# Kernel tuning notes

Measured on AMD Instinct MI355X. Metric: run time of the kernel, lower is better.

Reference implementation:

```python
import jax, jax.numpy as jnp
import numpy as np

B, S, DIN, DH = 8, 8192, 256, 256


def setup_inputs() -> dict:
    key = jax.random.key(0)
    k0, k1, k2, k3, k4 = jax.random.split(key, 5)
    stdv = 1.0 / np.sqrt(DIN)
    x = jax.random.normal(k0, (B, S, DIN), jnp.float32)
    W0 = jax.random.uniform(k1, (2 * DH, DIN), jnp.float32, -stdv, stdv)
    b0 = jax.random.uniform(k2, (2 * DH,), jnp.float32, -stdv, stdv)
    stdv2 = 1.0 / np.sqrt(DH)
    W1 = jax.random.uniform(k3, (2 * DH, DH), jnp.float32, -stdv2, stdv2)
    b1 = jax.random.uniform(k4, (2 * DH,), jnp.float32, -stdv2, stdv2)
    return {"x": x, "W0": W0, "b0": b0, "W1": W1, "b1": b1}


def _log_g(x):
    # log of g(x) = x + 0.5 for x >= 0 else sigmoid(x)
    return jnp.where(x >= 0, jnp.log(jax.nn.relu(x) + 0.5), -jax.nn.softplus(-x))


def _mingru_layer(x, W, b):
    # x: (B,S,Din); W: (2*DH, Din); b: (2*DH,)
    gh = jnp.einsum('bsd,ed->bse', x, W) + b          # (B,S,2*DH)
    gate, hidden = jnp.split(gh, 2, axis=-1)          # each (B,S,DH)
    log_coeffs = -jax.nn.softplus(gate)               # log(1 - z)
    log_vals = -jax.nn.softplus(-gate) + _log_g(hidden)  # log z + log h_tilde
    Bb, Ss, Dd = log_coeffs.shape
    # initial hidden h0 = g(0) = 0.5  ->  log(h0) = log(0.5)
    log_h0 = jnp.full((Bb, 1, Dd), jnp.log(0.5), log_coeffs.dtype)
    log_values = jnp.concatenate([log_h0, log_vals], axis=1)          # (B,S+1,DH)
    a_star = jnp.concatenate(
        [jnp.zeros((Bb, 1, Dd), log_coeffs.dtype), jnp.cumsum(log_coeffs, axis=1)],
        axis=1)                                                       # (B,S+1,DH)
    log_h = a_star + jax.lax.cumlogsumexp(log_values - a_star, axis=1)
    return jnp.exp(log_h)[:, 1:]                                      # (B,S,DH)


def reference(x, W0, b0, W1, b1):
    out0 = _mingru_layer(x, W0, b0)
    out1 = _mingru_layer(out0, W1, b1)
    h = jnp.stack([out0[:, -1:], out1[:, -1:]])  # (num_layers,B,1,DH)
    return out1, h
```

## Files before the change

kernel.cpp:

```cpp
#include <hip/hip_runtime.h>
#include <hip/hip_bf16.h>

#define Bb 8
#define Ss 8192
#define Dd 256
#define Mm (Bb * Ss)
#define Nn 512
#define NCHUNK 128
#define CLEN (Ss / NCHUNK)
#define TSP 68

typedef __hip_bfloat16 bf16;
typedef __attribute__((ext_vector_type(8))) short short8;
typedef __attribute__((ext_vector_type(4))) float f32x4;

__global__ __launch_bounds__(256) void cvt_weights(
    const float* __restrict__ inA, const float* __restrict__ inB,
    bf16* __restrict__ outA, bf16* __restrict__ outB, long n4each) {
  long i = (long)blockIdx.x * blockDim.x + threadIdx.x;
  const float* in = inA;
  bf16* out = outA;
  if (i >= n4each) {
    in = inB;
    out = outB;
    i -= n4each;
  }
  if (i >= n4each) return;
  const float4 v = ((const float4*)in)[i];
  union { ushort4 u; bf16 h[4]; } o;
  o.h[0] = __float2bfloat16(v.x);
  o.h[1] = __float2bfloat16(v.y);
  o.h[2] = __float2bfloat16(v.z);
  o.h[3] = __float2bfloat16(v.w);
  ((ushort4*)out)[i] = o.u;
}

__device__ __forceinline__ void av_from_gh(float gate, float hid, float& a,
                                           float& v) {
  const float eg = __expf(gate);
  a = __builtin_amdgcn_rcpf(1.f + eg);
  const float z = 1.f - a;
  const float eh = __expf(fminf(hid, 0.f));
  const float sig = eh * __builtin_amdgcn_rcpf(1.f + eh);
  const float gfun = (hid >= 0.f) ? (hid + 0.5f) : sig;
  v = z * gfun;
}

__device__ __forceinline__ unsigned pack_av(float a, float v) {
  union { bf16 h[2]; unsigned u; } o;
  o.h[0] = __float2bfloat16(a);
  o.h[1] = __float2bfloat16(v);
  return o.u;
}

template <bool F32A>
__global__ __launch_bounds__(256, 3) void gemm_av_fused(
    const void* __restrict__ Xv, const bf16* __restrict__ W,
    const float* __restrict__ bias, unsigned* __restrict__ AV,
    float2* __restrict__ AVs) {
  __shared__ __align__(16) char sm[32768];
  bf16* Ab[2] = {(bf16*)sm, (bf16*)(sm + 8192)};
  bf16* Bbf[2] = {(bf16*)(sm + 16384), (bf16*)(sm + 24576)};
  unsigned* Ts = (unsigned*)sm;
  float2* Ps = (float2*)(sm + 20480);

  const int tid = threadIdx.x;
  const int w = tid >> 6;
  const int l = tid & 63;
  const int fl = l & 15;
  const int q = l >> 4;

  const int id = blockIdx.x;
  const int lin = ((id & 7) << 8) | (id >> 3);
  const int cb = lin & 3;
  const int bt = lin >> 2;
  const long rowBase = (long)bt * 128;
  const int wrow = (w >> 1) * 64;
  const int wc = (w & 1) * 32;

  const float* Xf = (const float*)Xv;
  const bf16* Xb = (const bf16*)Xv;

  const float* aSF[2];
  const bf16* aSB[2];
  const bf16* bS[2];
  int ldsOff[2];
#pragma unroll
  for (int c = 0; c < 2; c++) {
    const int idx = c * 256 + tid;
    const int row = idx >> 2;
    const int kq = idx & 3;
    ldsOff[c] = row * 32 + (kq ^ ((row >> 1) & 3)) * 8;
    aSF[c] = Xf + (rowBase + row) * 256 + kq * 8;
    aSB[c] = Xb + (rowBase + row) * 256 + kq * 8;
    const int grow = (row < 64) ? (cb * 64 + row) : (192 + cb * 64 + row);
    bS[c] = W + (long)grow * 256 + kq * 8;
  }

  short8 aReg[2], bReg[2];
  float4 aF[2][2];

  auto loadG = [&](int ks) {
    if constexpr (F32A) {
#pragma unroll
      for (int c = 0; c < 2; c++) {
        aF[c][0] = *(const float4*)(aSF[c] + ks * 32);
        aF[c][1] = *(const float4*)(aSF[c] + ks * 32 + 4);
      }
    } else {
#pragma unroll
      for (int c = 0; c < 2; c++)
        aReg[c] = *(const short8*)(aSB[c] + ks * 32);
    }
#pragma unroll
    for (int c = 0; c < 2; c++)
      bReg[c] = *(const short8*)(bS[c] + ks * 32);
  };
  auto writeL = [&](int bi) {
#pragma unroll
    for (int c = 0; c < 2; c++) {
      short8 av_;
      if constexpr (F32A) {
        const float vals[8] = {aF[c][0].x, aF[c][0].y, aF[c][0].z, aF[c][0].w,
                               aF[c][1].x, aF[c][1].y, aF[c][1].z, aF[c][1].w};
#pragma unroll
        for (int i = 0; i < 8; i++) {
          union { bf16 h; short s; } t;
          t.h = __float2bfloat16(vals[i]);
          av_[i] = t.s;
        }
      } else {
        av_ = aReg[c];
      }
      *(short8*)(Ab[bi] + ldsOff[c]) = av_;
    }
#pragma unroll
    for (int c = 0; c < 2; c++)
      *(short8*)(Bbf[bi] + ldsOff[c]) = bReg[c];
  };

  int aOff[4], bOff[4];
#pragma unroll
  for (int mt = 0; mt < 4; mt++) {
    const int row = wrow + 16 * mt + fl;
    aOff[mt] = row * 32 + (q ^ ((row >> 1) & 3)) * 8;
  }
#pragma unroll
  for (int nt = 0; nt < 4; nt++) {
    const int row =
        (nt < 2) ? (wc + 16 * nt + fl) : (64 + wc + 16 * (nt - 2) + fl);
    bOff[nt] = row * 32 + (q ^ ((row >> 1) & 3)) * 8;
  }

  f32x4 acc[4][4];
#pragma unroll
  for (int i = 0; i < 4; i++)
#pragma unroll
    for (int j = 0; j < 4; j++) acc[i][j] = (f32x4)0.0f;

  loadG(0);
  writeL(0);
  loadG(1);
  __syncthreads();
#pragma unroll
  for (int ks = 0; ks < 8; ks++) {
    const int bi = ks & 1;
    short8 af[4], bf_[4];
#pragma unroll
    for (int mt = 0; mt < 4; mt++)
      af[mt] = *(const short8*)(Ab[bi] + aOff[mt]);
#pragma unroll
    for (int nt = 0; nt < 4; nt++)
      bf_[nt] = *(const short8*)(Bbf[bi] + bOff[nt]);
    if (ks < 7) writeL(bi ^ 1);
    if (ks < 6) loadG(ks + 2);
#pragma unroll
    for (int mt = 0; mt < 4; mt++)
#pragma unroll
      for (int nt = 0; nt < 4; nt++)
        acc[mt][nt] = __builtin_amdgcn_mfma_f32_16x16x32_bf16(
            af[mt], bf_[nt], acc[mt][nt], 0, 0, 0);
    asm volatile("s_waitcnt lgkmcnt(0)" ::: "memory");
    __builtin_amdgcn_s_barrier();
  }

  float bg[2], bh[2];
#pragma unroll
  for (int p = 0; p < 2; p++) {
    const int d = cb * 64 + wc + 16 * p + fl;
    bg[p] = bias[d];
    bh[p] = bias[256 + d];
  }
  unsigned pk[4][2][4];
#pragma unroll
  for (int mt = 0; mt < 4; mt++)
#pragma unroll
    for (int p = 0; p < 2; p++)
#pragma unroll
      for (int r = 0; r < 4; r++) {
        float a, v;
        av_from_gh(acc[mt][p][r] + bg[p], acc[mt][p + 2][r] + bh[p], a, v);
        pk[mt][p][r] = pack_av(a, v);
      }

#pragma unroll
  for (int h = 0; h < 2; h++) {
    if ((w >> 1) == h) {
#pragma unroll
      for (int mt = 0; mt < 4; mt++)
#pragma unroll
        for (int p = 0; p < 2; p++)
#pragma unroll
          for (int r = 0; r < 4; r++)
            Ts[(16 * mt + 4 * q + r) * TSP + wc + 16 * p + fl] = pk[mt][p][r];
    }
    __syncthreads();
    {
      unsigned* dst = AV + ((long)cb * Mm + rowBase + h * 64) * 64;
#pragma unroll
      for (int j = 0; j < 4; j++) {
        const int idx = j * 256 + tid;
        const int t = idx >> 4;
        const int d4 = idx & 15;
        const uint4 val = *(const uint4*)(Ts + t * TSP + d4 * 4);
        *(uint4*)(dst + 4 * idx) = val;
      }
    }
    {
      const int dl = tid & 63;
      const int sg = tid >> 6;
      float A = 1.f, H = 0.f;
#pragma unroll
      for (int t = 0; t < 16; t++) {
        const unsigned p = Ts[(sg * 16 + t) * TSP + dl];
        const float a = __uint_as_float((p & 0xffffu) << 16);
        const float v = __uint_as_float(p & 0xffff0000u);
        A *= a;
        H = a * H + v;
      }
      Ps[sg * 64 + dl] = make_float2(A, H);
    }
    __syncthreads();
    if (tid < 64) {
      float2 r = Ps[tid];
#pragma unroll
      for (int s = 1; s < 4; s++) {
        const float2 n = Ps[s * 64 + tid];
        r = make_float2(r.x * n.x, n.x * r.y + n.y);
      }
      const long cg = (long)(bt >> 6) * NCHUNK + ((bt & 63) << 1) + h;
      AVs[cg * 256 + cb * 64 + tid] = r;
    }
    __syncthreads();
  }
}

template <bool WRITE_BF16>
__global__ __launch_bounds__(256) void scan_final(
    const unsigned* __restrict__ AV, const float2* __restrict__ AVs,
    bf16* __restrict__ OutB, float* __restrict__ OutF,
    float* __restrict__ Hlast) {
  const int d = threadIdx.x;
  const int c = blockIdx.x % NCHUNK;
  const int b = blockIdx.x / NCHUNK;

  float h = 0.5f;
#pragma unroll 4
  for (int j = 0; j < c; j++) {
    const float2 av = AVs[((long)b * NCHUNK + j) * 256 + d];
    h = av.x * h + av.y;
  }

  const long row0 = (long)b * Ss + (long)c * CLEN;
  const unsigned* src = AV + (long)(d >> 6) * Mm * 64 + (d & 63);
  long obase = row0 * 256 + d;
#pragma unroll 8
  for (int t = 0; t < CLEN; t++) {
    const unsigned p = src[(row0 + t) * 64];
    const float a = __uint_as_float((p & 0xffffu) << 16);
    const float v = __uint_as_float(p & 0xffff0000u);
    h = a * h + v;
    if (WRITE_BF16)
      OutB[obase] = __float2bfloat16(h);
    else
      OutF[obase] = h;
    obase += 256;
  }
  if (c == NCHUNK - 1) Hlast[b * 256 + d] = h;
}

extern "C" void kernel_launch(void* const* d_in, const int* in_sizes, int n_in,
                              void* d_out, int out_size, void* d_ws,
                              size_t ws_size, hipStream_t stream) {
  const float* x = (const float*)d_in[0];
  const float* W0f = (const float*)d_in[1];
  const float* b0 = (const float*)d_in[2];
  const float* W1f = (const float*)d_in[3];
  const float* b1 = (const float*)d_in[4];

  float* outF = (float*)d_out;
  float* hlast = outF + (long)Mm * 256;
  bf16* X1b = (bf16*)d_out;

  char* ws = (char*)d_ws;
  unsigned* AV = (unsigned*)ws;
  bf16* W0b = (bf16*)(ws + (long)Mm * 256 * 4);
  bf16* W1b = W0b + (long)Nn * Dd;
  float2* AVs = (float2*)(W1b + (long)Nn * Dd);

  const dim3 gemmGrid(2048);
  const dim3 blk(256);

  const long n4w = (long)Nn * Dd / 4;
  cvt_weights<<<dim3((2 * n4w + 255) / 256), blk, 0, stream>>>(W0f, W1f, W0b,
                                                               W1b, n4w);

  gemm_av_fused<true><<<gemmGrid, blk, 0, stream>>>(x, W0b, b0, AV, AVs);
  scan_final<true><<<dim3(Bb * NCHUNK), blk, 0, stream>>>(AV, AVs, X1b,
                                                          nullptr, hlast);

  gemm_av_fused<false><<<gemmGrid, blk, 0, stream>>>(X1b, W1b, b1, AV, AVs);
  scan_final<false><<<dim3(Bb * NCHUNK), blk, 0, stream>>>(
      AV, AVs, nullptr, outF, hlast + Bb * 256);
}
```

Baseline: 242.2 us.

## Fuse weight bf16 conversion into GEMM and deepen prefetch for layer two

Removes the separate weight-conversion kernel launch. Each GEMM block now loads fp32 weights and converts them to bf16 while writing to LDS. Adds a DEPTH template so the second-layer GEMM prefetches three k-steps ahead using double register staging. In exchange, every block reloads fp32 weights, which is twice the bytes of bf16, and does redundant conversions. The deeper staging raises register pressure, which could hurt occupancy at 3 waves/SIMD.

```diff
diff --git a/kernel.cpp b/kernel.cpp
--- a/kernel.cpp
+++ b/kernel.cpp
@@ -13,27 +13,6 @@
 typedef __hip_bfloat16 bf16;
 typedef __attribute__((ext_vector_type(8))) short short8;
 typedef __attribute__((ext_vector_type(4))) float f32x4;
-
-__global__ __launch_bounds__(256) void cvt_weights(
-    const float* __restrict__ inA, const float* __restrict__ inB,
-    bf16* __restrict__ outA, bf16* __restrict__ outB, long n4each) {
-  long i = (long)blockIdx.x * blockDim.x + threadIdx.x;
-  const float* in = inA;
-  bf16* out = outA;
-  if (i >= n4each) {
-    in = inB;
-    out = outB;
-    i -= n4each;
-  }
-  if (i >= n4each) return;
-  const float4 v = ((const float4*)in)[i];
-  union { ushort4 u; bf16 h[4]; } o;
-  o.h[0] = __float2bfloat16(v.x);
-  o.h[1] = __float2bfloat16(v.y);
-  o.h[2] = __float2bfloat16(v.z);
-  o.h[3] = __float2bfloat16(v.w);
-  ((ushort4*)out)[i] = o.u;
-}
 
 __device__ __forceinline__ void av_from_gh(float gate, float hid, float& a,
                                            float& v) {
@@ -53,9 +32,21 @@
   return o.u;
 }
 
-template <bool F32A>
+__device__ __forceinline__ short8 cvt8(const float4& u0, const float4& u1) {
+  const float vals[8] = {u0.x, u0.y, u0.z, u0.w, u1.x, u1.y, u1.z, u1.w};
+  short8 r;
+#pragma unroll
+  for (int i = 0; i < 8; i++) {
+    union { bf16 h; short s; } t;
+    t.h = __float2bfloat16(vals[i]);
+    r[i] = t.s;
+  }
+  return r;
+}
+
+template <bool F32A, int DEPTH>
 __global__ __launch_bounds__(256, 3) void gemm_av_fused(
-    const void* __restrict__ Xv, const bf16* __restrict__ W,
+    const void* __restrict__ Xv, const float* __restrict__ Wf,
     const float* __restrict__ bias, unsigned* __restrict__ AV,
     float2* __restrict__ AVs) {
   __shared__ __align__(16) char sm[32768];
@@ -83,7 +74,7 @@
 
   const float* aSF[2];
   const bf16* aSB[2];
-  const bf16* bS[2];
+  const float* bSF[2];
   int ldsOff[2];
 #pragma unroll
   for (int c = 0; c < 2; c++) {
@@ -94,49 +85,44 @@
     aSF[c] = Xf + (rowBase + row) * 256 + kq * 8;
     aSB[c] = Xb + (rowBase + row) * 256 + kq * 8;
     const int grow = (row < 64) ? (cb * 64 + row) : (192 + cb * 64 + row);
-    bS[c] = W + (long)grow * 256 + kq * 8;
-  }
-
-  short8 aReg[2], bReg[2];
-  float4 aF[2][2];
-
-  auto loadG = [&](int ks) {
+    bSF[c] = Wf + (long)grow * 256 + kq * 8;
+  }
+
+  short8 aReg[2][2];
+  float4 aF[2][2][2];
+  float4 bF[2][2][2];
+
+  auto loadG = [&](int rs, int ks) {
     if constexpr (F32A) {
 #pragma unroll
       for (int c = 0; c < 2; c++) {
-        aF[c][0] = *(const float4*)(aSF[c] + ks * 32);
-        aF[c][1] = *(const float4*)(aSF[c] + ks * 32 + 4);
+        aF[rs][c][0] = *(const float4*)(aSF[c] + ks * 32);
+        aF[rs][c][1] = *(const float4*)(aSF[c] + ks * 32 + 4);
       }
     } else {
 #pragma unroll
       for (int c = 0; c < 2; c++)
-        aReg[c] = *(const short8*)(aSB[c] + ks * 32);
-    }
-#pragma unroll
-    for (int c = 0; c < 2; c++)
-      bReg[c] = *(const short8*)(bS[c] + ks * 32);
+        aReg[rs][c] = *(const short8*)(aSB[c] + ks * 32);
+    }
+#pragma unroll
+    for (int c = 0; c < 2; c++) {
+      bF[rs][c][0] = *(const float4*)(bSF[c] + ks * 32);
+      bF[rs][c][1] = *(const float4*)(bSF[c] + ks * 32 + 4);
+    }
   };
-  auto writeL = [&](int bi) {
+  auto writeL = [&](int bi, int rs) {
 #pragma unroll
     for (int c = 0; c < 2; c++) {
       short8 av_;
-      if constexpr (F32A) {
-        const float vals[8] = {aF[c][0].x, aF[c][0].y, aF[c][0].z, aF[c][0].w,
-                               aF[c][1].x, aF[c][1].y, aF[c][1].z, aF[c][1].w};
-#pragma unroll
-        for (int i = 0; i < 8; i++) {
-          union { bf16 h; short s; } t;
-          t.h = __float2bfloat16(vals[i]);
-          av_[i] = t.s;
-        }
-      } else {
-        av_ = aReg[c];
-      }
+      if constexpr (F32A)
+        av_ = cvt8(aF[rs][c][0], aF[rs][c][1]);
+      else
+        av_ = aReg[rs][c];
       *(short8*)(Ab[bi] + ldsOff[c]) = av_;
     }
 #pragma unroll
     for (int c = 0; c < 2; c++)
-      *(short8*)(Bbf[bi] + ldsOff[c]) = bReg[c];
+      *(short8*)(Bbf[bi] + ldsOff[c]) = cvt8(bF[rs][c][0], bF[rs][c][1]);
   };
 
   int aOff[4], bOff[4];
@@ -158,9 +144,16 @@
 #pragma unroll
     for (int j = 0; j < 4; j++) acc[i][j] = (f32x4)0.0f;
 
-  loadG(0);
-  writeL(0);
-  loadG(1);
+  if constexpr (DEPTH == 2) {
+    loadG(0, 0);
+    writeL(0, 0);
+    loadG(0, 1);
+  } else {
+    loadG(0, 0);
+    writeL(0, 0);
+    loadG(1, 1);
+    loadG(0, 2);
+  }
   __syncthreads();
 #pragma unroll
   for (int ks = 0; ks < 8; ks++) {
@@ -172,8 +165,14 @@
 #pragma unroll
     for (int nt = 0; nt < 4; nt++)
       bf_[nt] = *(const short8*)(Bbf[bi] + bOff[nt]);
-    if (ks < 7) writeL(bi ^ 1);
-    if (ks < 6) loadG(ks + 2);
+    if constexpr (DEPTH == 2) {
+      if (ks < 7) writeL(bi ^ 1, 0);
+      if (ks < 6) loadG(0, ks + 2);
+    } else {
+      const int rs = (ks + 1) & 1;
+      if (ks < 7) writeL(bi ^ 1, rs);
+      if (ks < 5) loadG(rs, ks + 3);
+    }
 #pragma unroll
     for (int mt = 0; mt < 4; mt++)
 #pragma unroll
@@ -304,22 +303,17 @@
 
   char* ws = (char*)d_ws;
   unsigned* AV = (unsigned*)ws;
-  bf16* W0b = (bf16*)(ws + (long)Mm * 256 * 4);
-  bf16* W1b = W0b + (long)Nn * Dd;
-  float2* AVs = (float2*)(W1b + (long)Nn * Dd);
+  float2* AVs = (float2*)(ws + (long)Mm * 256 * 4);
 
   const dim3 gemmGrid(2048);
   const dim3 blk(256);
 
-  const long n4w = (long)Nn * Dd / 4;
-  cvt_weights<<<dim3((2 * n4w + 255) / 256), blk, 0, stream>>>(W0f, W1f, W0b,
-                                                               W1b, n4w);
-
-  gemm_av_fused<true><<<gemmGrid, blk, 0, stream>>>(x, W0b, b0, AV, AVs);
+  gemm_av_fused<true, 2><<<gemmGrid, blk, 0, stream>>>(x, W0f, b0, AV, AVs);
   scan_final<true><<<dim3(Bb * NCHUNK), blk, 0, stream>>>(AV, AVs, X1b,
                                                           nullptr, hlast);
 
-  gemm_av_fused<false><<<gemmGrid, blk, 0, stream>>>(X1b, W1b, b1, AV, AVs);
+  gemm_av_fused<false, 3><<<gemmGrid, blk, 0, stream>>>(X1b, W1f, b1, AV,
+                                                        AVs);
   scan_final<false><<<dim3(Bb * NCHUNK), blk, 0, stream>>>(
       AV, AVs, nullptr, outF, hlast + Bb * 256);
 }
```

Result: slower. 253.3 us (+4.6%).
